# Kernel optimization log

Hardware: AMD Instinct MI355X
Metric: run time of the kernel (lower is better)

Reference implementation:

```python
import jax, jax.numpy as jnp
import numpy as np

EPS = 1e-5

def _conv1x1(x, w, b):
    # x: (b,c,h,w), w: (o,c) -> (b,o,h,w)
    return jnp.einsum('bchw,oc->bohw', x, w) + b[None, :, None, None]

def _maxpool2(x):
    b, c, h, w = x.shape
    return x.reshape(b, c, h // 2, 2, w // 2, 2).max(axis=(3, 5))

def setup_inputs() -> dict:
    key = jax.random.key(0)
    ks = jax.random.split(key, 11)
    C, CI, H, W, B = 256, 128, 64, 64, 8
    s = 0.05
    return {
        'x': jax.random.normal(ks[0], (B, C, H, W), jnp.float32),
        'Wg': jax.random.normal(ks[1], (CI, C), jnp.float32) * s,
        'bg': jax.random.normal(ks[2], (CI,), jnp.float32) * s,
        'Wt': jax.random.normal(ks[3], (CI, C), jnp.float32) * s,
        'bt': jax.random.normal(ks[4], (CI,), jnp.float32) * s,
        'Wp': jax.random.normal(ks[5], (CI, C), jnp.float32) * s,
        'bp': jax.random.normal(ks[6], (CI,), jnp.float32) * s,
        'Ww': jax.random.normal(ks[7], (C, CI), jnp.float32) * s,
        'bw': jax.random.normal(ks[8], (C,), jnp.float32) * s,
        'gamma': jax.random.normal(ks[9], (C,), jnp.float32),
        'beta': jax.random.normal(ks[10], (C,), jnp.float32),
    }

def reference(x, Wg, bg, Wt, bt, Wp, bp, Ww, bw, gamma, beta):
    b, C, H, W = x.shape
    CI = Wg.shape[0]
    # g and phi are sub-sampled by 2x2 max pool -> M = (H/2)*(W/2); theta keeps N = H*W
    g_x = _maxpool2(_conv1x1(x, Wg, bg)).reshape(b, CI, -1).transpose(0, 2, 1)   # (b,M,ci)
    theta_x = _conv1x1(x, Wt, bt).reshape(b, CI, -1).transpose(0, 2, 1)          # (b,N,ci)
    phi_x = _maxpool2(_conv1x1(x, Wp, bp)).reshape(b, CI, -1)                    # (b,ci,M)
    f = jnp.einsum('bnc,bcm->bnm', theta_x, phi_x)                               # (b,N,M)
    f_div_C = jax.nn.softmax(f, axis=-1)
    y = jnp.einsum('bnm,bmc->bnc', f_div_C, g_x)                                 # (b,N,ci)
    y = y.transpose(0, 2, 1).reshape(b, CI, H, W)
    # W: 1x1 conv + BatchNorm2d (training mode: batch statistics, biased var)
    wy = _conv1x1(y, Ww, bw)
    mean = wy.mean(axis=(0, 2, 3), keepdims=True)
    var = ((wy - mean) ** 2).mean(axis=(0, 2, 3), keepdims=True)
    wy = (wy - mean) * jax.lax.rsqrt(var + EPS)
    wy = wy * gamma[None, :, None, None] + beta[None, :, None, None]
    z = wy + x
    # self.avg_pool is AdaptiveMaxPool2d(1): global spatial max
    return z.max(axis=(2, 3), keepdims=True)
```

## Files before the change

### kernel.cpp

```cpp
#include <hip/hip_runtime.h>
#include <hip/hip_bf16.h>
#include <stdint.h>

using f32x4  = __attribute__((ext_vector_type(4))) float;
using bf16x8 = __attribute__((ext_vector_type(8))) short;
using short4v = __attribute__((ext_vector_type(4))) short;

#define DEVINL static __device__ __forceinline__

DEVINL short f2bf(float f) {
    union { float f; uint32_t u; } v; v.f = f;
    uint32_t r = (v.u + 0x7FFFu + ((v.u >> 16) & 1u)) >> 16;
    return (short)(uint16_t)r;
}
DEVINL float bf2f(short s) {
    union { uint32_t u; float f; } v; v.u = ((uint32_t)(uint16_t)s) << 16;
    return v.f;
}
DEVINL float fexp2(float x) {
    float r;
    asm("v_exp_f32 %0, %1" : "=v"(r) : "v"(x));
    return r;
}
DEVINL uint32_t pk2bf(float a, float b) {
    union { __hip_bfloat162 v; uint32_t u; } c;
    c.v = __float22bfloat162_rn(float2{a, b});
    return c.u;
}

DEVINL void gld16(const short* g, short* l) {
    __builtin_amdgcn_global_load_lds(
        (const __attribute__((address_space(1))) unsigned int*)g,
        (__attribute__((address_space(3))) unsigned int*)l, 16, 0, 0);
}

#define LOG2E 1.44269504f

__global__ __launch_bounds__(256) void k0_prep(
        const float* __restrict__ Wg, const float* __restrict__ Wt, const float* __restrict__ Wp,
        const float* __restrict__ bg, const float* __restrict__ bt, const float* __restrict__ bp,
        const float* __restrict__ Ww,
        short* __restrict__ W_all, short* __restrict__ Ww16, float* __restrict__ b_all) {
    int i = blockIdx.x * 256 + threadIdx.x;
    if (i < 384 * 256) {
        int r = i >> 8, c = i & 255;
        float v = (r < 128) ? Wg[r * 256 + c]
                : (r < 256) ? Wt[(r - 128) * 256 + c] * LOG2E
                            : Wp[(r - 256) * 256 + c];
        W_all[i] = f2bf(v);
    } else if (i < 384 * 256 + 256 * 128) {
        int j = i - 384 * 256;
        Ww16[j] = f2bf(Ww[j]);
    }
    if (i < 384) {
        b_all[i] = (i < 128) ? bg[i] : (i < 256) ? bt[i - 128] * LOG2E : bp[i - 256];
    }
}

__global__ __launch_bounds__(256) void k1_conv(const float* __restrict__ x,
        const short* __restrict__ W_all, const float* __restrict__ b_all,
        short* __restrict__ OutT, short* __restrict__ Kmat, short* __restrict__ Vmat) {
    __shared__ short xs[128 * 32];
    __shared__ short obuf[128 * 128];
    const int ntile = blockIdx.x;
    const int b     = blockIdx.y;
    const int tid  = threadIdx.x;
    const int lane = tid & 63;
    const int wave = tid >> 6;
    const int wn = wave >> 1, wo = wave & 1;
    const int l15 = lane & 15, lh = lane >> 4;

    f32x4 acc[3][4][4];
    #pragma unroll
    for (int ot = 0; ot < 3; ot++)
        #pragma unroll
        for (int i = 0; i < 4; i++)
            #pragma unroll
            for (int j = 0; j < 4; j++) acc[ot][i][j] = f32x4{0.f, 0.f, 0.f, 0.f};

    const int n0 = ntile * 128;
    const float* xb = x + (size_t)b * 256 * 4096;

    const int srow_base = (lane & 15) + wave * 16;
    const int sc0 = (lane >> 4) * 8;

    for (int kt = 0; kt < 8; kt++) {
        __syncthreads();
        #pragma unroll
        for (int p = 0; p < 2; p++) {
            int row = srow_base + p * 64;
            const float* xp = xb + (size_t)(kt * 32 + sc0) * 4096 + n0 + row;
            bf16x8 w8;
            #pragma unroll
            for (int j = 0; j < 8; j++) w8[j] = f2bf(xp[(size_t)j * 4096]);
            int ch = (sc0 >> 3) ^ ((row >> 1) & 3);
            *(bf16x8*)&xs[row * 32 + ch * 8] = w8;
        }
        __syncthreads();

        bf16x8 a[4];
        #pragma unroll
        for (int nf = 0; nf < 4; nf++) {
            int row = wn * 64 + nf * 16 + l15;
            int ch  = lh ^ ((row >> 1) & 3);
            a[nf] = *(const bf16x8*)&xs[row * 32 + ch * 8];
        }
        #pragma unroll
        for (int ot = 0; ot < 3; ot++) {
            bf16x8 w[4];
            #pragma unroll
            for (int of = 0; of < 4; of++)
                w[of] = *(const bf16x8*)(W_all + (size_t)(ot * 128 + wo * 64 + of * 16 + l15) * 256 + kt * 32 + lh * 8);
            #pragma unroll
            for (int nf = 0; nf < 4; nf++)
                #pragma unroll
                for (int of = 0; of < 4; of++)
                    acc[ot][nf][of] = __builtin_amdgcn_mfma_f32_16x16x32_bf16(a[nf], w[of], acc[ot][nf][of], 0, 0, 0);
        }
    }

    #pragma unroll
    for (int ot = 0; ot < 3; ot++) {
        __syncthreads();
        #pragma unroll
        for (int of = 0; of < 4; of++) {
            int ocol = wo * 64 + of * 16 + l15;
            float bias = b_all[ot * 128 + ocol];
            #pragma unroll
            for (int nf = 0; nf < 4; nf++)
                #pragma unroll
                for (int r = 0; r < 4; r++) {
                    int n  = wn * 64 + nf * 16 + lh * 4 + r;
                    int ch = (ocol >> 3) ^ (n & 15);
                    obuf[n * 128 + ch * 8 + (ocol & 7)] = f2bf(acc[ot][nf][of][r] + bias);
                }
        }
        __syncthreads();

        if (ot == 1) {
            #pragma unroll
            for (int p = 0; p < 8; p++) {
                int n  = wave * 4 + lh + p * 16;
                int ch = l15 ^ (n & 15);
                bf16x8 v = *(const bf16x8*)&obuf[n * 128 + ch * 8];
                *(bf16x8*)(OutT + ((size_t)b * 4096 + n0 + n) * 128 + l15 * 8) = v;
            }
        } else if (ot == 2) {
            const int wp = tid >> 3;
            const int cc = (tid & 7) * 16;
            short* kdst = Kmat + ((size_t)b * 1024 + ntile * 32 + wp) * 128 + cc;
            #pragma unroll
            for (int cblk = 0; cblk < 2; cblk++) {
                const int chunk = (cc >> 3) + cblk;
                float mx[8];
                #pragma unroll
                for (int j = 0; j < 8; j++) mx[j] = -1e30f;
                #pragma unroll
                for (int q4 = 0; q4 < 4; q4++) {
                    int n = (q4 >> 1) * 64 + 2 * wp + (q4 & 1);
                    bf16x8 v = *(const bf16x8*)&obuf[n * 128 + ((chunk ^ (n & 15)) * 8)];
                    #pragma unroll
                    for (int j = 0; j < 8; j++) mx[j] = fmaxf(mx[j], bf2f(v[j]));
                }
                bf16x8 vo;
                #pragma unroll
                for (int j = 0; j < 8; j++) vo[j] = f2bf(mx[j]);
                *(bf16x8*)(kdst + cblk * 8) = vo;
            }
        } else {
            const int c   = tid >> 1;
            const int wp0 = (tid & 1) * 16;
            const int chb = c >> 3, cl = c & 7;
            #pragma unroll
            for (int half = 0; half < 2; half++) {
                bf16x8 vo;
                #pragma unroll
                for (int j = 0; j < 8; j++) {
                    int wp = wp0 + half * 8 + j;
                    float mx = -1e30f;
                    #pragma unroll
                    for (int q4 = 0; q4 < 4; q4++) {
                        int n = (q4 >> 1) * 64 + 2 * wp + (q4 & 1);
                        mx = fmaxf(mx, bf2f(obuf[n * 128 + ((chb ^ (n & 15)) * 8) + cl]));
                    }
                    vo[j] = f2bf(mx);
                }
                *(bf16x8*)(Vmat + ((size_t)b * 128 + c) * 1024 + ntile * 32 + wp0 + half * 8) = vo;
            }
        }
    }
}

__global__ __launch_bounds__(256) void k3_attn(const short* __restrict__ OutT,
        const short* __restrict__ Kmat, const short* __restrict__ Vmat,
        const short* __restrict__ Ww16, const float* __restrict__ bw,
        short* __restrict__ wy) {
    __shared__ short smem[36864];
    short* const sKb = smem;
    short* const sVb = smem + 16384;
    short* const sPb = smem + 32768;

    const int bid = blockIdx.x;
    const int b   = bid & 7;
    const int nt  = bid >> 3;
    const int tid = threadIdx.x;
    const int lane = tid & 63;
    const int wave = tid >> 6;
    const int l15 = lane & 15, lh = lane >> 4;
    const int nblk = nt * 64;
    const int n0 = nblk + wave * 16;

    const short* Kb = Kmat + (size_t)b * 1024 * 128;
    const short* Vb = Vmat + (size_t)b * 128 * 1024;
    short* sPw = sPb + wave * 1024;

    auto STAGE = [&](int t, int bufi) {
        const int m0 = t * 64;
        #pragma unroll
        for (int i = 0; i < 4; i++) {
            const int segb = (i * 4 + wave) * 64;
            const int rowK = (segb >> 4) + (lane >> 4);
            const int chkK = lane & 15;
            gld16(Kb + (size_t)(m0 + rowK) * 128 + ((chkK ^ (rowK & 15)) << 3),
                  sKb + bufi * 8192 + segb * 8);
            const int rowV = (segb >> 3) + (lane >> 3);
            const int chkV = lane & 7;
            gld16(Vb + (size_t)rowV * 1024 + m0 + ((chkV ^ (rowV & 7)) << 3),
                  sVb + bufi * 8192 + segb * 8);
        }
    };

    bf16x8 q[4];
    {
        const short* qrow = OutT + ((size_t)b * 4096 + n0 + l15) * 128;
        #pragma unroll
        for (int ks = 0; ks < 4; ks++)
            q[ks] = *(const bf16x8*)(qrow + ks * 32 + lh * 8);
    }

    f32x4 y[8];
    #pragma unroll
    for (int cf = 0; cf < 8; cf++) y[cf] = f32x4{0.f, 0.f, 0.f, 0.f};
    float mrun = -1e30f, lrun = 0.f;

    STAGE(0, 0);
    int cur = 0;

    for (int t = 0; t < 16; t++) {
        if (t < 15) {
            STAGE(t + 1, cur ^ 1);
            asm volatile("s_waitcnt vmcnt(8)" ::: "memory");
        } else {
            asm volatile("s_waitcnt vmcnt(0)" ::: "memory");
        }
        __builtin_amdgcn_s_barrier();
        __builtin_amdgcn_sched_barrier(0);

        const short* cK = sKb + cur * 8192;
        const short* cV = sVb + cur * 8192;

        f32x4 S[4];
        #pragma unroll
        for (int mf = 0; mf < 4; mf++) S[mf] = f32x4{0.f, 0.f, 0.f, 0.f};
        #pragma unroll
        for (int ks = 0; ks < 4; ks++) {
            bf16x8 kf[4];
            #pragma unroll
            for (int mf = 0; mf < 4; mf++) {
                int mrow = mf * 16 + l15;
                int jj   = ks * 4 + lh;
                kf[mf] = *(const bf16x8*)&cK[mrow * 128 + ((jj ^ (mrow & 15)) << 3)];
            }
            __builtin_amdgcn_s_setprio(1);
            #pragma unroll
            for (int mf = 0; mf < 4; mf++)
                S[mf] = __builtin_amdgcn_mfma_f32_16x16x32_bf16(kf[mf], q[ks], S[mf], 0, 0, 0);
            __builtin_amdgcn_s_setprio(0);
        }

        float pm = S[0][0];
        #pragma unroll
        for (int mf = 0; mf < 4; mf++)
            #pragma unroll
            for (int r = 0; r < 4; r++) pm = fmaxf(pm, S[mf][r]);
        pm = fmaxf(pm, __shfl_xor(pm, 16));
        pm = fmaxf(pm, __shfl_xor(pm, 32));

        if (__any(pm > mrun + 8.656f)) {
            float mnew  = fmaxf(mrun, pm);
            float alpha = fexp2(mrun - mnew);
            mrun = mnew;
            lrun *= alpha;
            float aR[4];
            #pragma unroll
            for (int r = 0; r < 4; r++) aR[r] = __shfl(alpha, lh * 4 + r);
            #pragma unroll
            for (int cf = 0; cf < 8; cf++)
                #pragma unroll
                for (int r = 0; r < 4; r++) y[cf][r] *= aR[r];
        }
        float rs = 0.f;
        #pragma unroll
        for (int mf = 0; mf < 4; mf++)
            #pragma unroll
            for (int r = 0; r < 4; r++) {
                float p = fexp2(S[mf][r] - mrun);
                S[mf][r] = p;
                rs += p;
            }
        rs += __shfl_xor(rs, 16);
        rs += __shfl_xor(rs, 32);
        lrun += rs;

        #pragma unroll
        for (int mf = 0; mf < 4; mf++) {
            uint2 pk = { pk2bf(S[mf][0], S[mf][1]), pk2bf(S[mf][2], S[mf][3]) };
            *(uint2*)&sPw[(l15 << 6) + (((mf * 4 + lh) ^ l15) << 2)] = pk;
        }

        #pragma unroll
        for (int ks2 = 0; ks2 < 2; ks2++) {
            int u0 = ks2 * 8 + lh * 2;
            short4v lo = *(const short4v*)&sPw[(l15 << 6) + (((u0)     ^ l15) << 2)];
            short4v hi = *(const short4v*)&sPw[(l15 << 6) + (((u0 + 1) ^ l15) << 2)];
            bf16x8 pa = { lo.x, lo.y, lo.z, lo.w, hi.x, hi.y, hi.z, hi.w };
            int jj = ks2 * 4 + lh;
            __builtin_amdgcn_s_setprio(1);
            #pragma unroll
            for (int cf = 0; cf < 8; cf++) {
                int crow = cf * 16 + l15;
                bf16x8 vf = *(const bf16x8*)&cV[crow * 64 + ((jj ^ (crow & 7)) << 3)];
                y[cf] = __builtin_amdgcn_mfma_f32_16x16x32_bf16(pa, vf, y[cf], 0, 0, 0);
            }
            __builtin_amdgcn_s_setprio(0);
        }

        __builtin_amdgcn_sched_barrier(0);
        __builtin_amdgcn_s_barrier();
        cur ^= 1;
    }

    float linv[4];
    #pragma unroll
    for (int r = 0; r < 4; r++) linv[r] = 1.f / __shfl(lrun, lh * 4 + r);

    short* const Yt = smem;
    #pragma unroll
    for (int cf = 0; cf < 8; cf++) {
        int c = cf * 16 + l15;
        #pragma unroll
        for (int r = 0; r < 4; r++) {
            int n = wave * 16 + lh * 4 + r;
            Yt[n * 128 + (((c >> 3) ^ (n & 15)) << 3) + (c & 7)] = f2bf(y[cf][r] * linv[r]);
        }
    }
    __syncthreads();

    bf16x8 by[4][4];
    #pragma unroll
    for (int nf = 0; nf < 4; nf++)
        #pragma unroll
        for (int ks = 0; ks < 4; ks++) {
            int n  = nf * 16 + l15;
            int kc = ks * 4 + lh;
            by[nf][ks] = *(const bf16x8*)&Yt[n * 128 + ((kc ^ (n & 15)) << 3)];
        }

    short* const sOut = smem + 8192 + wave * 4608;
    const int obase = wave * 64;
    #pragma unroll
    for (int of = 0; of < 4; of++) {
        bf16x8 aw[4];
        #pragma unroll
        for (int ks = 0; ks < 4; ks++)
            aw[ks] = *(const bf16x8*)(Ww16 + (size_t)(obase + of * 16 + l15) * 128 + ks * 32 + lh * 8);
        #pragma unroll
        for (int nf = 0; nf < 4; nf++) {
            f32x4 acc = f32x4{0.f, 0.f, 0.f, 0.f};
            #pragma unroll
            for (int ks = 0; ks < 4; ks++)
                acc = __builtin_amdgcn_mfma_f32_16x16x32_bf16(aw[ks], by[nf][ks], acc, 0, 0, 0);
            #pragma unroll
            for (int r = 0; r < 4; r++) {
                int o_loc = of * 16 + lh * 4 + r;
                sOut[o_loc * 72 + nf * 16 + l15] = f2bf(acc[r] + bw[obase + o_loc]);
            }
        }
    }

    #pragma unroll
    for (int p = 0; p < 8; p++) {
        int o_loc = p * 8 + (lane >> 3);
        int n8    = (lane & 7) * 8;
        bf16x8 v = *(const bf16x8*)&sOut[o_loc * 72 + n8];
        *(bf16x8*)(wy + ((size_t)b * 256 + obase + o_loc) * 4096 + nblk + n8) = v;
    }
}

__global__ __launch_bounds__(512) void k45_bnmax(const short* __restrict__ wy,
        const float* __restrict__ x,
        const float* __restrict__ gamma, const float* __restrict__ beta,
        float* __restrict__ outp) {
    const int o   = blockIdx.x;
    const int tid = threadIdx.x;
    const int lane = tid & 63;
    const int wave = tid >> 6;

    bf16x8 w8[8];
    float s = 0.f, s2 = 0.f;
    #pragma unroll
    for (int b = 0; b < 8; b++) {
        w8[b] = *(const bf16x8*)(wy + ((size_t)b * 256 + o) * 4096 + tid * 8);
        #pragma unroll
        for (int j = 0; j < 8; j++) {
            float f = bf2f(w8[b][j]);
            s += f; s2 += f * f;
        }
    }
    #pragma unroll
    for (int off = 1; off < 64; off <<= 1) { s += __shfl_xor(s, off); s2 += __shfl_xor(s2, off); }
    __shared__ float sred[8][2];
    if (lane == 0) { sred[wave][0] = s; sred[wave][1] = s2; }
    __syncthreads();
    s = 0.f; s2 = 0.f;
    #pragma unroll
    for (int wv = 0; wv < 8; wv++) { s += sred[wv][0]; s2 += sred[wv][1]; }
    float mean = s * (1.f / 32768.f);
    float var  = s2 * (1.f / 32768.f) - mean * mean;
    float rstd = rsqrtf(var + 1e-5f);
    float A = rstd * gamma[o];
    float B = beta[o] - mean * A;

    float mx[8];
    #pragma unroll
    for (int b = 0; b < 8; b++) {
        const float* px = x + ((size_t)b * 256 + o) * 4096 + tid * 8;
        float4 xa = *(const float4*)px;
        float4 xb = *(const float4*)(px + 4);
        float m = bf2f(w8[b][0]) * A + B + xa.x;
        m = fmaxf(m, bf2f(w8[b][1]) * A + B + xa.y);
        m = fmaxf(m, bf2f(w8[b][2]) * A + B + xa.z);
        m = fmaxf(m, bf2f(w8[b][3]) * A + B + xa.w);
        m = fmaxf(m, bf2f(w8[b][4]) * A + B + xb.x);
        m = fmaxf(m, bf2f(w8[b][5]) * A + B + xb.y);
        m = fmaxf(m, bf2f(w8[b][6]) * A + B + xb.z);
        m = fmaxf(m, bf2f(w8[b][7]) * A + B + xb.w);
        mx[b] = m;
    }
    #pragma unroll
    for (int b = 0; b < 8; b++)
        #pragma unroll
        for (int off = 1; off < 64; off <<= 1) mx[b] = fmaxf(mx[b], __shfl_xor(mx[b], off));
    __shared__ float mred[8][8];
    if (lane == 0) {
        #pragma unroll
        for (int b = 0; b < 8; b++) mred[wave][b] = mx[b];
    }
    __syncthreads();
    if (tid < 8) {
        float m = mred[0][tid];
        #pragma unroll
        for (int wv = 1; wv < 8; wv++) m = fmaxf(m, mred[wv][tid]);
        outp[tid * 256 + o] = m;
    }
}

extern "C" void kernel_launch(void* const* d_in, const int* in_sizes, int n_in,
                              void* d_out, int out_size, void* d_ws, size_t ws_size,
                              hipStream_t stream) {
    const float* x     = (const float*)d_in[0];
    const float* Wg    = (const float*)d_in[1];
    const float* bg    = (const float*)d_in[2];
    const float* Wt    = (const float*)d_in[3];
    const float* bt    = (const float*)d_in[4];
    const float* Wp    = (const float*)d_in[5];
    const float* bp    = (const float*)d_in[6];
    const float* Ww    = (const float*)d_in[7];
    const float* bw    = (const float*)d_in[8];
    const float* gamma = (const float*)d_in[9];
    const float* beta  = (const float*)d_in[10];
    float* outp = (float*)d_out;

    char* ws = (char*)d_ws;
    size_t off = 0;
    auto alloc = [&](size_t bytes) -> void* {
        void* p = ws + off;
        off = (off + bytes + 255) & ~(size_t)255;
        return p;
    };
    short* W_all = (short*)alloc((size_t)384 * 256 * 2);
    short* Ww16  = (short*)alloc((size_t)256 * 128 * 2);
    float* b_all = (float*)alloc((size_t)384 * 4);
    short* OutT  = (short*)alloc((size_t)8 * 4096 * 128 * 2);
    short* Kmat  = (short*)alloc((size_t)8 * 1024 * 128 * 2);
    short* Vmat  = (short*)alloc((size_t)8 * 128 * 1024 * 2);
    short* wy    = (short*)alloc((size_t)8 * 256 * 4096 * 2);

    k0_prep<<<512, 256, 0, stream>>>(Wg, Wt, Wp, bg, bt, bp, Ww, W_all, Ww16, b_all);
    k1_conv<<<dim3(32, 8), 256, 0, stream>>>(x, W_all, b_all, OutT, Kmat, Vmat);
    k3_attn<<<512, 256, 0, stream>>>(OutT, Kmat, Vmat, Ww16, bw, wy);
    k45_bnmax<<<256, 512, 0, stream>>>(wy, x, gamma, beta, outp);
}
```

Baseline: 85.51 us.

## Split attention keys across two wave groups and double query rows per wave

The attention kernel now uses 512-thread blocks covering 128 query rows. Two halves of the block each process half of the 1024 keys (split-K flash attention), and each wave handles 32 query rows instead of 16, so every K/V fragment loaded from LDS feeds twice as many MFMAs. The two partial softmax states are merged through shared memory before the output projection, which is done in two 64-row passes. This cuts K/V staging traffic per query and the sequential loop length, but adds an LDS merge step, extra barriers, higher register pressure, and half as many blocks.

```diff
diff --git a/kernel.cpp b/kernel.cpp
--- a/kernel.cpp
+++ b/kernel.cpp
@@ -191,63 +191,66 @@
     }
 }
 
-__global__ __launch_bounds__(256) void k3_attn(const short* __restrict__ OutT,
+__global__ __launch_bounds__(512) void k3_attn(const short* __restrict__ OutT,
         const short* __restrict__ Kmat, const short* __restrict__ Vmat,
         const short* __restrict__ Ww16, const float* __restrict__ bw,
         short* __restrict__ wy) {
-    __shared__ short smem[36864];
-    short* const sKb = smem;
-    short* const sVb = smem + 16384;
-    short* const sPb = smem + 32768;
-
+    __shared__ short smem[65536];
     const int bid = blockIdx.x;
     const int b   = bid & 7;
     const int nt  = bid >> 3;
     const int tid = threadIdx.x;
     const int lane = tid & 63;
     const int wave = tid >> 6;
+    const int half = wave >> 2;
+    const int wl   = wave & 3;
     const int l15 = lane & 15, lh = lane >> 4;
-    const int nblk = nt * 64;
-    const int n0 = nblk + wave * 16;
+    const int nblk = nt * 128;
+    const int n0 = nblk + wl * 32;
+    const int mbase = half * 512;
 
     const short* Kb = Kmat + (size_t)b * 1024 * 128;
     const short* Vb = Vmat + (size_t)b * 128 * 1024;
-    short* sPw = sPb + wave * 1024;
+    short* const sKh = smem + half * 16384;
+    short* const sVh = smem + 32768 + half * 16384;
 
     auto STAGE = [&](int t, int bufi) {
-        const int m0 = t * 64;
+        const int m0 = mbase + t * 64;
         #pragma unroll
         for (int i = 0; i < 4; i++) {
-            const int segb = (i * 4 + wave) * 64;
+            const int segb = (i * 4 + wl) * 64;
             const int rowK = (segb >> 4) + (lane >> 4);
             const int chkK = lane & 15;
             gld16(Kb + (size_t)(m0 + rowK) * 128 + ((chkK ^ (rowK & 15)) << 3),
-                  sKb + bufi * 8192 + segb * 8);
+                  sKh + bufi * 8192 + segb * 8);
             const int rowV = (segb >> 3) + (lane >> 3);
             const int chkV = lane & 7;
             gld16(Vb + (size_t)rowV * 1024 + m0 + ((chkV ^ (rowV & 7)) << 3),
-                  sVb + bufi * 8192 + segb * 8);
+                  sVh + bufi * 8192 + segb * 8);
         }
     };
 
-    bf16x8 q[4];
-    {
-        const short* qrow = OutT + ((size_t)b * 4096 + n0 + l15) * 128;
+    bf16x8 q[2][4];
+    #pragma unroll
+    for (int nf = 0; nf < 2; nf++) {
+        const short* qrow = OutT + ((size_t)b * 4096 + n0 + nf * 16 + l15) * 128;
         #pragma unroll
         for (int ks = 0; ks < 4; ks++)
-            q[ks] = *(const bf16x8*)(qrow + ks * 32 + lh * 8);
-    }
-
-    f32x4 y[8];
-    #pragma unroll
-    for (int cf = 0; cf < 8; cf++) y[cf] = f32x4{0.f, 0.f, 0.f, 0.f};
-    float mrun = -1e30f, lrun = 0.f;
+            q[nf][ks] = *(const bf16x8*)(qrow + ks * 32 + lh * 8);
+    }
+
+    f32x4 y[2][8];
+    #pragma unroll
+    for (int nf = 0; nf < 2; nf++)
+        #pragma unroll
+        for (int cf = 0; cf < 8; cf++) y[nf][cf] = f32x4{0.f, 0.f, 0.f, 0.f};
+    float mrun[2] = { -1e30f, -1e30f }, lrun[2] = { 0.f, 0.f };
 
     STAGE(0, 0);
     int cur = 0;
 
-    for (int t = 0; t < 16; t++) {
-        if (t < 15) {
+    for (int t = 0; t < 8; t++) {
+        if (t < 7) {
             STAGE(t + 1, cur ^ 1);
             asm volatile("s_waitcnt vmcnt(8)" ::: "memory");
         } else {
@@ -256,12 +259,14 @@
         __builtin_amdgcn_s_barrier();
         __builtin_amdgcn_sched_barrier(0);
 
-        const short* cK = sKb + cur * 8192;
-        const short* cV = sVb + cur * 8192;
-
-        f32x4 S[4];
-        #pragma unroll
-        for (int mf = 0; mf < 4; mf++) S[mf] = f32x4{0.f, 0.f, 0.f, 0.f};
+        const short* cK = sKh + cur * 8192;
+        const short* cV = sVh + cur * 8192;
+
+        f32x4 S[2][4];
+        #pragma unroll
+        for (int nf = 0; nf < 2; nf++)
+            #pragma unroll
+            for (int mf = 0; mf < 4; mf++) S[nf][mf] = f32x4{0.f, 0.f, 0.f, 0.f};
         #pragma unroll
         for (int ks = 0; ks < 4; ks++) {
             bf16x8 kf[4];
@@ -273,64 +278,91 @@
             }
             __builtin_amdgcn_s_setprio(1);
             #pragma unroll
+            for (int nf = 0; nf < 2; nf++)
+                #pragma unroll
+                for (int mf = 0; mf < 4; mf++)
+                    S[nf][mf] = __builtin_amdgcn_mfma_f32_16x16x32_bf16(kf[mf], q[nf][ks], S[nf][mf], 0, 0, 0);
+            __builtin_amdgcn_s_setprio(0);
+        }
+
+        float pm[2];
+        #pragma unroll
+        for (int nf = 0; nf < 2; nf++) {
+            float v = S[nf][0][0];
+            #pragma unroll
             for (int mf = 0; mf < 4; mf++)
-                S[mf] = __builtin_amdgcn_mfma_f32_16x16x32_bf16(kf[mf], q[ks], S[mf], 0, 0, 0);
-            __builtin_amdgcn_s_setprio(0);
-        }
-
-        float pm = S[0][0];
-        #pragma unroll
-        for (int mf = 0; mf < 4; mf++)
-            #pragma unroll
-            for (int r = 0; r < 4; r++) pm = fmaxf(pm, S[mf][r]);
-        pm = fmaxf(pm, __shfl_xor(pm, 16));
-        pm = fmaxf(pm, __shfl_xor(pm, 32));
-
-        if (__any(pm > mrun + 8.656f)) {
-            float mnew  = fmaxf(mrun, pm);
-            float alpha = fexp2(mrun - mnew);
-            mrun = mnew;
-            lrun *= alpha;
-            float aR[4];
-            #pragma unroll
-            for (int r = 0; r < 4; r++) aR[r] = __shfl(alpha, lh * 4 + r);
-            #pragma unroll
-            for (int cf = 0; cf < 8; cf++)
-                #pragma unroll
-                for (int r = 0; r < 4; r++) y[cf][r] *= aR[r];
-        }
-        float rs = 0.f;
-        #pragma unroll
-        for (int mf = 0; mf < 4; mf++)
-            #pragma unroll
-            for (int r = 0; r < 4; r++) {
-                float p = fexp2(S[mf][r] - mrun);
-                S[mf][r] = p;
-                rs += p;
-            }
-        rs += __shfl_xor(rs, 16);
-        rs += __shfl_xor(rs, 32);
-        lrun += rs;
-
-        #pragma unroll
-        for (int mf = 0; mf < 4; mf++) {
-            uint2 pk = { pk2bf(S[mf][0], S[mf][1]), pk2bf(S[mf][2], S[mf][3]) };
-            *(uint2*)&sPw[(l15 << 6) + (((mf * 4 + lh) ^ l15) << 2)] = pk;
-        }
+                #pragma unroll
+                for (int r = 0; r < 4; r++) v = fmaxf(v, S[nf][mf][r]);
+            v = fmaxf(v, __shfl_xor(v, 16));
+            v = fmaxf(v, __shfl_xor(v, 32));
+            pm[nf] = v;
+        }
+        bool grow = (pm[0] > mrun[0] + 8.656f) | (pm[1] > mrun[1] + 8.656f);
+        if (__any(grow)) {
+            #pragma unroll
+            for (int nf = 0; nf < 2; nf++) {
+                float mnew  = fmaxf(mrun[nf], pm[nf]);
+                float alpha = fexp2(mrun[nf] - mnew);
+                mrun[nf] = mnew;
+                lrun[nf] *= alpha;
+                float aR[4];
+                #pragma unroll
+                for (int r = 0; r < 4; r++) aR[r] = __shfl(alpha, lh * 4 + r);
+                #pragma unroll
+                for (int cf = 0; cf < 8; cf++)
+                    #pragma unroll
+                    for (int r = 0; r < 4; r++) y[nf][cf][r] *= aR[r];
+            }
+        }
+        #pragma unroll
+        for (int nf = 0; nf < 2; nf++) {
+            float rs = 0.f;
+            #pragma unroll
+            for (int mf = 0; mf < 4; mf++)
+                #pragma unroll
+                for (int r = 0; r < 4; r++) {
+                    float p = fexp2(S[nf][mf][r] - mrun[nf]);
+                    S[nf][mf][r] = p;
+                    rs += p;
+                }
+            rs += __shfl_xor(rs, 16);
+            rs += __shfl_xor(rs, 32);
+            lrun[nf] += rs;
+        }
+
+        __builtin_amdgcn_sched_barrier(0);
+        __builtin_amdgcn_s_barrier();
+
+        short* const sPw = sKh + cur * 8192 + wl * 2048;
+        #pragma unroll
+        for (int nf = 0; nf < 2; nf++)
+            #pragma unroll
+            for (int mf = 0; mf < 4; mf++) {
+                uint2 pk = { pk2bf(S[nf][mf][0], S[nf][mf][1]), pk2bf(S[nf][mf][2], S[nf][mf][3]) };
+                int row = nf * 16 + l15;
+                *(uint2*)&sPw[(row << 6) + (((mf * 4 + lh) ^ l15) << 2)] = pk;
+            }
 
         #pragma unroll
         for (int ks2 = 0; ks2 < 2; ks2++) {
             int u0 = ks2 * 8 + lh * 2;
-            short4v lo = *(const short4v*)&sPw[(l15 << 6) + (((u0)     ^ l15) << 2)];
-            short4v hi = *(const short4v*)&sPw[(l15 << 6) + (((u0 + 1) ^ l15) << 2)];
-            bf16x8 pa = { lo.x, lo.y, lo.z, lo.w, hi.x, hi.y, hi.z, hi.w };
+            bf16x8 pa[2];
+            #pragma unroll
+            for (int nf = 0; nf < 2; nf++) {
+                int row = nf * 16 + l15;
+                short4v lo = *(const short4v*)&sPw[(row << 6) + (((u0)     ^ l15) << 2)];
+                short4v hi = *(const short4v*)&sPw[(row << 6) + (((u0 + 1) ^ l15) << 2)];
+                pa[nf] = bf16x8{ lo.x, lo.y, lo.z, lo.w, hi.x, hi.y, hi.z, hi.w };
+            }
             int jj = ks2 * 4 + lh;
             __builtin_amdgcn_s_setprio(1);
             #pragma unroll
             for (int cf = 0; cf < 8; cf++) {
                 int crow = cf * 16 + l15;
                 bf16x8 vf = *(const bf16x8*)&cV[crow * 64 + ((jj ^ (crow & 7)) << 3)];
-                y[cf] = __builtin_amdgcn_mfma_f32_16x16x32_bf16(pa, vf, y[cf], 0, 0, 0);
+                #pragma unroll
+                for (int nf = 0; nf < 2; nf++)
+                    y[nf][cf] = __builtin_amdgcn_mfma_f32_16x16x32_bf16(pa[nf], vf, y[nf][cf], 0, 0, 0);
             }
             __builtin_amdgcn_s_setprio(0);
         }
@@ -340,60 +372,109 @@
         cur ^= 1;
     }
 
-    float linv[4];
-    #pragma unroll
-    for (int r = 0; r < 4; r++) linv[r] = 1.f / __shfl(lrun, lh * 4 + r);
+    float* const fsm = (float*)smem;
+    float* const fl  = fsm + 128 * 132;
+    float* const fm  = fl + 128;
+    if (half == 1) {
+        #pragma unroll
+        for (int nf = 0; nf < 2; nf++) {
+            #pragma unroll
+            for (int cf = 0; cf < 8; cf++)
+                #pragma unroll
+                for (int r = 0; r < 4; r++)
+                    fsm[(wl * 32 + nf * 16 + lh * 4 + r) * 132 + cf * 16 + l15] = y[nf][cf][r];
+            if (lh == 0) {
+                fl[wl * 32 + nf * 16 + l15] = lrun[nf];
+                fm[wl * 32 + nf * 16 + l15] = mrun[nf];
+            }
+        }
+    }
+    __syncthreads();
+    if (half == 0) {
+        #pragma unroll
+        for (int nf = 0; nf < 2; nf++) {
+            float m1 = fm[wl * 32 + nf * 16 + l15];
+            float l1 = fl[wl * 32 + nf * 16 + l15];
+            float mnew = fmaxf(mrun[nf], m1);
+            float a0 = fexp2(mrun[nf] - mnew);
+            float a1 = fexp2(m1 - mnew);
+            float lnew = lrun[nf] * a0 + l1 * a1;
+            float aR0[4], aR1[4], li[4];
+            #pragma unroll
+            for (int r = 0; r < 4; r++) {
+                aR0[r] = __shfl(a0, lh * 4 + r);
+                aR1[r] = __shfl(a1, lh * 4 + r);
+                li[r]  = 1.f / __shfl(lnew, lh * 4 + r);
+            }
+            #pragma unroll
+            for (int cf = 0; cf < 8; cf++)
+                #pragma unroll
+                for (int r = 0; r < 4; r++) {
+                    float y1 = fsm[(wl * 32 + nf * 16 + lh * 4 + r) * 132 + cf * 16 + l15];
+                    y[nf][cf][r] = (y[nf][cf][r] * aR0[r] + y1 * aR1[r]) * li[r];
+                }
+        }
+    }
+    __syncthreads();
 
     short* const Yt = smem;
     #pragma unroll
-    for (int cf = 0; cf < 8; cf++) {
-        int c = cf * 16 + l15;
-        #pragma unroll
-        for (int r = 0; r < 4; r++) {
-            int n = wave * 16 + lh * 4 + r;
-            Yt[n * 128 + (((c >> 3) ^ (n & 15)) << 3) + (c & 7)] = f2bf(y[cf][r] * linv[r]);
-        }
-    }
-    __syncthreads();
-
-    bf16x8 by[4][4];
-    #pragma unroll
-    for (int nf = 0; nf < 4; nf++)
-        #pragma unroll
-        for (int ks = 0; ks < 4; ks++) {
-            int n  = nf * 16 + l15;
-            int kc = ks * 4 + lh;
-            by[nf][ks] = *(const bf16x8*)&Yt[n * 128 + ((kc ^ (n & 15)) << 3)];
-        }
-
-    short* const sOut = smem + 8192 + wave * 4608;
-    const int obase = wave * 64;
-    #pragma unroll
-    for (int of = 0; of < 4; of++) {
-        bf16x8 aw[4];
-        #pragma unroll
-        for (int ks = 0; ks < 4; ks++)
-            aw[ks] = *(const bf16x8*)(Ww16 + (size_t)(obase + of * 16 + l15) * 128 + ks * 32 + lh * 8);
-        #pragma unroll
-        for (int nf = 0; nf < 4; nf++) {
-            f32x4 acc = f32x4{0.f, 0.f, 0.f, 0.f};
+    for (int h = 0; h < 2; h++) {
+        if (h) __syncthreads();
+        if (half == 0 && (wl >> 1) == h) {
+            #pragma unroll
+            for (int nf = 0; nf < 2; nf++)
+                #pragma unroll
+                for (int cf = 0; cf < 8; cf++) {
+                    int c = cf * 16 + l15;
+                    #pragma unroll
+                    for (int r = 0; r < 4; r++) {
+                        int n = (wl & 1) * 32 + nf * 16 + lh * 4 + r;
+                        Yt[n * 128 + (((c >> 3) ^ (n & 15)) << 3) + (c & 7)] = f2bf(y[nf][cf][r]);
+                    }
+                }
+        }
+        __syncthreads();
+
+        bf16x8 by[4][4];
+        #pragma unroll
+        for (int nfi = 0; nfi < 4; nfi++)
+            #pragma unroll
+            for (int ks = 0; ks < 4; ks++) {
+                int n  = nfi * 16 + l15;
+                int kc = ks * 4 + lh;
+                by[nfi][ks] = *(const bf16x8*)&Yt[n * 128 + ((kc ^ (n & 15)) << 3)];
+            }
+
+        short* const sOut = smem + 8192 + wave * 2304;
+        const int obase = wave * 32;
+        #pragma unroll
+        for (int of = 0; of < 2; of++) {
+            bf16x8 aw[4];
             #pragma unroll
             for (int ks = 0; ks < 4; ks++)
-                acc = __builtin_amdgcn_mfma_f32_16x16x32_bf16(aw[ks], by[nf][ks], acc, 0, 0, 0);
-            #pragma unroll
-            for (int r = 0; r < 4; r++) {
-                int o_loc = of * 16 + lh * 4 + r;
-                sOut[o_loc * 72 + nf * 16 + l15] = f2bf(acc[r] + bw[obase + o_loc]);
-            }
-        }
-    }
-
-    #pragma unroll
-    for (int p = 0; p < 8; p++) {
-        int o_loc = p * 8 + (lane >> 3);
-        int n8    = (lane & 7) * 8;
-        bf16x8 v = *(const bf16x8*)&sOut[o_loc * 72 + n8];
-        *(bf16x8*)(wy + ((size_t)b * 256 + obase + o_loc) * 4096 + nblk + n8) = v;
+                aw[ks] = *(const bf16x8*)(Ww16 + (size_t)(obase + of * 16 + l15) * 128 + ks * 32 + lh * 8);
+            #pragma unroll
+            for (int nfi = 0; nfi < 4; nfi++) {
+                f32x4 acc = f32x4{0.f, 0.f, 0.f, 0.f};
+                #pragma unroll
+                for (int ks = 0; ks < 4; ks++)
+                    acc = __builtin_amdgcn_mfma_f32_16x16x32_bf16(aw[ks], by[nfi][ks], acc, 0, 0, 0);
+                #pragma unroll
+                for (int r = 0; r < 4; r++) {
+                    int o_loc = of * 16 + lh * 4 + r;
+                    sOut[o_loc * 72 + nfi * 16 + l15] = f2bf(acc[r] + bw[obase + o_loc]);
+                }
+            }
+        }
+
+        #pragma unroll
+        for (int p = 0; p < 4; p++) {
+            int o_loc = p * 8 + (lane >> 3);
+            int n8    = (lane & 7) * 8;
+            bf16x8 v = *(const bf16x8*)&sOut[o_loc * 72 + n8];
+            *(bf16x8*)(wy + ((size_t)b * 256 + obase + o_loc) * 4096 + nblk + h * 64 + n8) = v;
+        }
     }
 }
 
@@ -498,6 +579,6 @@
 
     k0_prep<<<512, 256, 0, stream>>>(Wg, Wt, Wp, bg, bt, bp, Ww, W_all, Ww16, b_all);
     k1_conv<<<dim3(32, 8), 256, 0, stream>>>(x, W_all, b_all, OutT, Kmat, Vmat);
-    k3_attn<<<512, 256, 0, stream>>>(OutT, Kmat, Vmat, Ww16, bw, wy);
+    k3_attn<<<256, 512, 0, stream>>>(OutT, Kmat, Vmat, Ww16, bw, wy);
     k45_bnmax<<<256, 512, 0, stream>>>(wy, x, gamma, beta, outp);
 }
```

New measurement: 85.57 us. About the same (+0.1%).
